# Performance work log

Hardware: AMD Instinct MI355X
Metric: run time of the kernel (lower is better)

Reference implementation:

```python
import jax, jax.numpy as jnp
import numpy as np

B = 262144          # batch of sample points
L = 16              # hash levels
T = 1 << 19         # hash table size per level
F = 2               # features per level
BASE_RES = 16
FINEST_RES = 512
DH = 64             # density MLP hidden
DOUT = 16           # density MLP out (density_out dim)
CH = 64             # color MLP hidden
PRIMES = np.array([1, 2654435761, 805459861], dtype=np.uint32)
_b = np.exp((np.log(FINEST_RES) - np.log(BASE_RES)) / (L - 1))
RES = jnp.asarray(np.floor(BASE_RES * _b ** np.arange(L)).astype(np.float32))  # (L,)


def _linear_init(key, fan_in, fan_out):
    kw, kb = jax.random.split(key)
    bound = 1.0 / np.sqrt(fan_in)
    w = jax.random.uniform(kw, (fan_in, fan_out), minval=-bound, maxval=bound)
    b = jax.random.uniform(kb, (fan_out,), minval=-bound, maxval=bound)
    return w, b


def setup_inputs() -> dict:
    key = jax.random.key(0)
    ks = jax.random.split(key, 10)
    coords = jax.random.uniform(ks[0], (B, 3), dtype=jnp.float32)          # in [0,1]
    directions = jax.random.normal(ks[1], (B, 3), dtype=jnp.float32)
    embeddings = jax.random.uniform(ks[2], (L, T, F), minval=-1e-4, maxval=1e-4, dtype=jnp.float32)
    dw1, db1 = _linear_init(ks[3], L * F, DH)
    dw2, db2 = _linear_init(ks[4], DH, DOUT)
    cw1, cb1 = _linear_init(ks[5], 16 + DOUT, CH)
    cw2, cb2 = _linear_init(ks[6], CH, CH)
    cw3, cb3 = _linear_init(ks[7], CH, CH)
    cw4, cb4 = _linear_init(ks[8], CH, 3)
    return dict(coords=coords, directions=directions, embeddings=embeddings,
                dw1=dw1, db1=db1, dw2=dw2, db2=db2,
                cw1=cw1, cb1=cb1, cw2=cw2, cb2=cb2,
                cw3=cw3, cb3=cb3, cw4=cw4, cb4=cb4)


def hash_encode(coords, embeddings):
    # coords: (B,3) in [0,1]; embeddings: (L,T,F)
    pos = coords[:, None, :] * RES[None, :, None]            # (B,L,3)
    p0 = jnp.floor(pos)
    frac = pos - p0                                           # (B,L,3)
    p0 = p0.astype(jnp.uint32)
    corners = jnp.stack([p0, p0 + jnp.uint32(1)], axis=-1)    # (B,L,3,2)
    h_ax = corners * jnp.asarray(PRIMES)[None, None, :, None]  # uint32 wraparound
    hidx = (h_ax[:, :, 0, :, None, None]
            ^ h_ax[:, :, 1, None, :, None]
            ^ h_ax[:, :, 2, None, None, :])                   # (B,L,2,2,2)
    hidx = (hidx & jnp.uint32(T - 1)).reshape(coords.shape[0], L, 8).astype(jnp.int32)
    feats = embeddings[jnp.arange(L)[None, :, None], hidx]    # (B,L,8,F)
    wx = jnp.stack([1.0 - frac[..., 0], frac[..., 0]], -1)    # (B,L,2)
    wy = jnp.stack([1.0 - frac[..., 1], frac[..., 1]], -1)
    wz = jnp.stack([1.0 - frac[..., 2], frac[..., 2]], -1)
    w = (wx[:, :, :, None, None] * wy[:, :, None, :, None] * wz[:, :, None, None, :])
    w = w.reshape(coords.shape[0], L, 8)                      # (B,L,8)
    out = jnp.sum(feats * w[..., None], axis=2)               # (B,L,F)
    return out.reshape(coords.shape[0], L * F)


def sh_encode_deg4(d):
    # d: (B,3) unit directions in [-1,1]; degree-4 real SH basis (16 comps)
    x, y, z = d[:, 0], d[:, 1], d[:, 2]
    xx, yy, zz = x * x, y * y, z * z
    xy, yz, xz = x * y, y * z, x * z
    c = jnp.full_like(x, 0.28209479177387814)
    return jnp.stack([
        c,
        -0.48860251190291987 * y,
        0.48860251190291987 * z,
        -0.48860251190291987 * x,
        1.0925484305920792 * xy,
        -1.0925484305920792 * yz,
        0.94617469575755997 * zz - 0.31539156525251999,
        -1.0925484305920792 * xz,
        0.54627421529603959 * (xx - yy),
        0.59004358992664352 * y * (-3.0 * xx + yy),
        2.8906114426405538 * xy * z,
        0.45704579946446572 * y * (1.0 - 5.0 * zz),
        0.3731763325901154 * z * (5.0 * zz - 3.0),
        0.45704579946446572 * x * (1.0 - 5.0 * zz),
        1.4453057213202769 * z * (xx - yy),
        0.59004358992664352 * x * (xx - 3.0 * yy),
    ], axis=1)


def reference(coords, directions, embeddings, dw1, db1, dw2, db2,
              cw1, cb1, cw2, cb2, cw3, cb3, cw4, cb4):
    # density net: hash encode -> Linear+ReLU -> Linear
    feat = hash_encode(coords, embeddings)                    # (B, L*F)
    h = jax.nn.relu(feat @ dw1 + db1)
    density_out = h @ dw2 + db2                               # (B, DOUT)
    density = jnp.exp(density_out[:, 0])                      # TruncExp fwd = exp
    # color net
    d = directions / jnp.linalg.norm(directions, axis=1, keepdims=True)
    d01 = (d + 1.0) / 2.0                                     # remap as in module
    sh = sh_encode_deg4(d01 * 2.0 - 1.0)                      # encoder maps back to [-1,1]
    inp = jnp.concatenate([sh, density_out], axis=1)          # (B, 32)
    x = jax.nn.relu(inp @ cw1 + cb1)
    x = jax.nn.relu(x @ cw2 + cb2)
    x = jax.nn.relu(x @ cw3 + cb3)
    color = jax.nn.sigmoid(x @ cw4 + cb4)                     # (B, 3)
    return density, color
```

## Files before the change

### kernel.cpp

```cpp
#include <hip/hip_runtime.h>
#include <cmath>

#define NPTS 262144
#define NLVL 16
#define TBL  524288u
#define TMASK 524287u
#define TPB  128

typedef __attribute__((ext_vector_type(8))) short short8;
typedef __attribute__((ext_vector_type(4))) float f32x4;

struct ResArr { float r[NLVL]; };

__device__ __forceinline__ unsigned short f2bf(float f) {
    union { float f; unsigned u; } v; v.f = f;
    unsigned r = v.u + 0x7FFFu + ((v.u >> 16) & 1u);
    return (unsigned short)(r >> 16);
}

#define MFMA(a,b,c) __builtin_amdgcn_mfma_f32_16x16x32_bf16((a),(b),(c),0,0,0)

__global__ __launch_bounds__(256) void hash_encode_k(
    const float* __restrict__ coords,
    const float* __restrict__ emb,
    unsigned* __restrict__ featws,
    ResArr res)
{
    const int b    = blockIdx.x;
    const int xcd  = b & 7;
    const int step = b >> 3;
    const int l    = (step < 1024) ? xcd : (xcd + 8);
    const int p    = (step & 1023) * 256 + threadIdx.x;

    const float cx = coords[3*p], cy = coords[3*p+1], cz = coords[3*p+2];
    const float r = res.r[l];

    const float px = cx*r, py = cy*r, pz = cz*r;
    const float fpx = floorf(px), fpy = floorf(py), fpz = floorf(pz);
    const float fx = px-fpx, fy = py-fpy, fz = pz-fpz;
    const unsigned ix=(unsigned)fpx, iy=(unsigned)fpy, iz=(unsigned)fpz;
    const unsigned hx0=ix,             hx1=ix+1u;
    const unsigned hy0=iy*2654435761u, hy1=(iy+1u)*2654435761u;
    const unsigned hz0=iz*805459861u,  hz1=(iz+1u)*805459861u;
    const unsigned base = (unsigned)l * TBL;

    const float2* __restrict__ emb2 = (const float2*)emb;
    const float2 f000 = emb2[base + ((hx0^hy0^hz0)&TMASK)];
    const float2 f001 = emb2[base + ((hx0^hy0^hz1)&TMASK)];
    const float2 f010 = emb2[base + ((hx0^hy1^hz0)&TMASK)];
    const float2 f011 = emb2[base + ((hx0^hy1^hz1)&TMASK)];
    const float2 f100 = emb2[base + ((hx1^hy0^hz0)&TMASK)];
    const float2 f101 = emb2[base + ((hx1^hy0^hz1)&TMASK)];
    const float2 f110 = emb2[base + ((hx1^hy1^hz0)&TMASK)];
    const float2 f111 = emb2[base + ((hx1^hy1^hz1)&TMASK)];

    const float wx0=1.f-fx, wy0=1.f-fy, wz0=1.f-fz;
    float o0, o1;
    o0 = wx0*wy0*wz0*f000.x;                 o1 = wx0*wy0*wz0*f000.y;
    o0 = fmaf(wx0*wy0*fz,  f001.x, o0);      o1 = fmaf(wx0*wy0*fz,  f001.y, o1);
    o0 = fmaf(wx0*fy*wz0,  f010.x, o0);      o1 = fmaf(wx0*fy*wz0,  f010.y, o1);
    o0 = fmaf(wx0*fy*fz,   f011.x, o0);      o1 = fmaf(wx0*fy*fz,   f011.y, o1);
    o0 = fmaf(fx*wy0*wz0,  f100.x, o0);      o1 = fmaf(fx*wy0*wz0,  f100.y, o1);
    o0 = fmaf(fx*wy0*fz,   f101.x, o0);      o1 = fmaf(fx*wy0*fz,   f101.y, o1);
    o0 = fmaf(fx*fy*wz0,   f110.x, o0);      o1 = fmaf(fx*fy*wz0,   f110.y, o1);
    o0 = fmaf(fx*fy*fz,    f111.x, o0);      o1 = fmaf(fx*fy*fz,    f111.y, o1);

    featws[(size_t)l * NPTS + p] = (unsigned)f2bf(o0) | ((unsigned)f2bf(o1) << 16);
}

__global__ __launch_bounds__(256, 3) void mlp_mfma_k(
    const unsigned* __restrict__ featws,
    const float* __restrict__ dirs,
    const float* __restrict__ dw1, const float* __restrict__ db1,
    const float* __restrict__ dw2, const float* __restrict__ db2,
    const float* __restrict__ cw1, const float* __restrict__ cb1,
    const float* __restrict__ cw2, const float* __restrict__ cb2,
    const float* __restrict__ cw3, const float* __restrict__ cb3,
    const float* __restrict__ cw4, const float* __restrict__ cb4,
    float* __restrict__ out)
{
    const int tid  = threadIdx.x;
    const int wid  = tid >> 6;
    const int lane = tid & 63;
    const int m16  = lane & 15;
    const int q    = lane >> 4;

    __shared__ __align__(16) unsigned short wlds[28 * 512];
    __shared__ float blds[288];
    __shared__ __align__(16) unsigned short featL[TPB * 40];
    __shared__ __align__(16) unsigned short actL[4 * 16 * 72];

    const unsigned char MAT[28] = {0,0,0,0, 1,1, 2,2,2,2, 3,3,3,3,3,3,3,3, 4,4,4,4,4,4,4,4, 5,5};
    const unsigned char K0 [28] = {0,0,0,0, 0,32, 0,0,0,0, 0,0,0,0,32,32,32,32, 0,0,0,0,32,32,32,32, 0,32};
    const unsigned char N0 [28] = {0,16,32,48, 0,0, 0,16,32,48, 0,16,32,48,0,16,32,48, 0,16,32,48,0,16,32,48, 0,0};

    #pragma unroll
    for (int s = 0; s < 28; ++s) {
        if ((s & 3) == wid) {
            const int mat = MAT[s];
            const float* src = mat==0?dw1 : mat==1?dw2 : mat==2?cw1 : mat==3?cw2 : mat==4?cw3 : cw4;
            const int fan = (mat==1) ? 16 : (mat==5) ? 3 : 64;
            const int k = (int)K0[s] + q*8;
            const int n = (int)N0[s] + m16;
            unsigned short u[8];
            #pragma unroll
            for (int j = 0; j < 8; ++j) {
                float v = 0.f;
                if (mat != 5 || n < 3) v = src[(k+j)*fan + n];
                u[j] = f2bf(v);
            }
            unsigned* w32 = (unsigned*)(wlds + s*512 + lane*8);
            w32[0] = (unsigned)u[0] | ((unsigned)u[1] << 16);
            w32[1] = (unsigned)u[2] | ((unsigned)u[3] << 16);
            w32[2] = (unsigned)u[4] | ((unsigned)u[5] << 16);
            w32[3] = (unsigned)u[6] | ((unsigned)u[7] << 16);
        }
    }
    {
        int t = tid;
        if      (t <  64) blds[t] = db1[t];
        else if (t <  80) blds[t] = db2[t-64];
        else if (t < 144) blds[t] = cb1[t-80];
        else if (t < 208) blds[t] = cb2[t-144];
    }
    if (tid < 80) {
        int t = tid + 208;
        if (t < 272) blds[t] = cb3[t-208];
        else         blds[t] = (t-272 < 3) ? cb4[t-272] : 0.f;
    }

    const int pbase = blockIdx.x * TPB;
    unsigned* fL32 = (unsigned*)featL;
    #pragma unroll
    for (int j = 0; j < 8; ++j) {
        const int idx  = j*256 + tid;
        const int l    = idx >> 7;
        const int ploc = idx & 127;
        fL32[ploc*20 + l] = featws[(size_t)l * NPTS + pbase + ploc];
    }
    __syncthreads();

    unsigned short* aw = actL + wid*1152;
    const short8* wfr = (const short8*)wlds;

    #pragma unroll
    for (int iter = 0; iter < 2; ++iter) {
        const int tile = wid + 4*iter;
        const int loc0 = tile*16;
        const int p0g  = pbase + loc0;

        short8 a0 = *(const short8*)(featL + (loc0+m16)*40 + q*8);
        f32x4 acc[4];
        #pragma unroll
        for (int nc = 0; nc < 4; ++nc) {
            const float b = blds[nc*16 + m16];
            acc[nc] = (f32x4){b,b,b,b};
            acc[nc] = MFMA(a0, wfr[nc*64 + lane], acc[nc]);
        }
        #pragma unroll
        for (int nc = 0; nc < 4; ++nc)
            #pragma unroll
            for (int r = 0; r < 4; ++r)
                aw[(q*4+r)*72 + nc*16 + m16] = f2bf(fmaxf(acc[nc][r], 0.f));

        short8 ad0 = *(const short8*)(aw + m16*72 + q*8);
        short8 ad1 = *(const short8*)(aw + m16*72 + 32 + q*8);
        f32x4 dob;
        { const float b = blds[64 + m16]; dob = (f32x4){b,b,b,b}; }
        dob = MFMA(ad0, wfr[4*64 + lane], dob);
        dob = MFMA(ad1, wfr[5*64 + lane], dob);

        if (m16 == 0) {
            #pragma unroll
            for (int r = 0; r < 4; ++r) out[p0g + q*4 + r] = expf(dob[r]);
        }

        #pragma unroll
        for (int r = 0; r < 4; ++r)
            aw[(q*4+r)*72 + 16 + m16] = f2bf(dob[r]);
        {
            const int pg = p0g + m16;
            const float dx0 = dirs[3*pg], dy0 = dirs[3*pg+1], dz0 = dirs[3*pg+2];
            const float inv = 1.f / sqrtf(dx0*dx0 + dy0*dy0 + dz0*dz0);
            float x = dx0*inv, y = dy0*inv, z = dz0*inv;
            x = ((x+1.f)*0.5f)*2.f - 1.f;
            y = ((y+1.f)*0.5f)*2.f - 1.f;
            z = ((z+1.f)*0.5f)*2.f - 1.f;
            float s0, s1, s2, s3;
            switch (q) {
            case 0: s0 = 0.28209479177387814f;
                    s1 = -0.48860251190291987f*y;
                    s2 =  0.48860251190291987f*z;
                    s3 = -0.48860251190291987f*x; break;
            case 1: s0 =  1.0925484305920792f*x*y;
                    s1 = -1.0925484305920792f*y*z;
                    s2 =  0.94617469575756f*z*z - 0.31539156525252f;
                    s3 = -1.0925484305920792f*x*z; break;
            case 2: s0 =  0.5462742152960396f*(x*x - y*y);
                    s1 =  0.5900435899266435f*y*(-3.f*x*x + y*y);
                    s2 =  2.890611442640554f*x*y*z;
                    s3 =  0.4570457994644657f*y*(1.f - 5.f*z*z); break;
            default:s0 =  0.3731763325901154f*z*(5.f*z*z - 3.f);
                    s1 =  0.4570457994644657f*x*(1.f - 5.f*z*z);
                    s2 =  1.445305721320277f*z*(x*x - y*y);
                    s3 =  0.5900435899266435f*x*(x*x - 3.f*y*y); break;
            }
            unsigned* ip = (unsigned*)(aw + m16*72 + q*4);
            ip[0] = (unsigned)f2bf(s0) | ((unsigned)f2bf(s1) << 16);
            ip[1] = (unsigned)f2bf(s2) | ((unsigned)f2bf(s3) << 16);
        }

        short8 ac0 = *(const short8*)(aw + m16*72 + q*8);
        #pragma unroll
        for (int nc = 0; nc < 4; ++nc) {
            const float b = blds[80 + nc*16 + m16];
            acc[nc] = (f32x4){b,b,b,b};
            acc[nc] = MFMA(ac0, wfr[(6+nc)*64 + lane], acc[nc]);
        }
        #pragma unroll
        for (int nc = 0; nc < 4; ++nc)
            #pragma unroll
            for (int r = 0; r < 4; ++r)
                aw[(q*4+r)*72 + nc*16 + m16] = f2bf(fmaxf(acc[nc][r], 0.f));

        short8 a20 = *(const short8*)(aw + m16*72 + q*8);
        short8 a21 = *(const short8*)(aw + m16*72 + 32 + q*8);
        #pragma unroll
        for (int nc = 0; nc < 4; ++nc) {
            const float b = blds[144 + nc*16 + m16];
            acc[nc] = (f32x4){b,b,b,b};
            acc[nc] = MFMA(a20, wfr[(10+nc)*64 + lane], acc[nc]);
            acc[nc] = MFMA(a21, wfr[(14+nc)*64 + lane], acc[nc]);
        }
        #pragma unroll
        for (int nc = 0; nc < 4; ++nc)
            #pragma unroll
            for (int r = 0; r < 4; ++r)
                aw[(q*4+r)*72 + nc*16 + m16] = f2bf(fmaxf(acc[nc][r], 0.f));

        short8 a30 = *(const short8*)(aw + m16*72 + q*8);
        short8 a31 = *(const short8*)(aw + m16*72 + 32 + q*8);
        #pragma unroll
        for (int nc = 0; nc < 4; ++nc) {
            const float b = blds[208 + nc*16 + m16];
            acc[nc] = (f32x4){b,b,b,b};
            acc[nc] = MFMA(a30, wfr[(18+nc)*64 + lane], acc[nc]);
            acc[nc] = MFMA(a31, wfr[(22+nc)*64 + lane], acc[nc]);
        }
        #pragma unroll
        for (int nc = 0; nc < 4; ++nc)
            #pragma unroll
            for (int r = 0; r < 4; ++r)
                aw[(q*4+r)*72 + nc*16 + m16] = f2bf(fmaxf(acc[nc][r], 0.f));

        short8 a40 = *(const short8*)(aw + m16*72 + q*8);
        short8 a41 = *(const short8*)(aw + m16*72 + 32 + q*8);
        f32x4 c4;
        { const float b = blds[272 + m16]; c4 = (f32x4){b,b,b,b}; }
        c4 = MFMA(a40, wfr[26*64 + lane], c4);
        c4 = MFMA(a41, wfr[27*64 + lane], c4);
        if (m16 < 3) {
            #pragma unroll
            for (int r = 0; r < 4; ++r)
                out[NPTS + 3*(p0g + q*4 + r) + m16] = 1.f / (1.f + expf(-c4[r]));
        }
    }
}

extern "C" void kernel_launch(void* const* d_in, const int* in_sizes, int n_in,
                              void* d_out, int out_size, void* d_ws, size_t ws_size,
                              hipStream_t stream)
{
    ResArr res;
    const double b = exp((log(512.0) - log(16.0)) / 15.0);
    for (int l = 0; l < NLVL; ++l)
        res.r[l] = (float)floor(16.0 * pow(b, (double)l));

    unsigned* featws = (unsigned*)d_ws;

    hash_encode_k<<<16384, 256, 0, stream>>>(
        (const float*)d_in[0],
        (const float*)d_in[2],
        featws, res);

    mlp_mfma_k<<<NPTS/TPB, 256, 0, stream>>>(
        featws,
        (const float*)d_in[1],
        (const float*)d_in[3],  (const float*)d_in[4],
        (const float*)d_in[5],  (const float*)d_in[6],
        (const float*)d_in[7],  (const float*)d_in[8],
        (const float*)d_in[9],  (const float*)d_in[10],
        (const float*)d_in[11], (const float*)d_in[12],
        (const float*)d_in[13], (const float*)d_in[14],
        (float*)d_out);
}
```

Measured before the change: 270.1 us.

## Densify coarse hash levels into linear grids for coalesced corner lookups

Adds a prepass kernel that copies the hashed embeddings for the first seven coarse levels into dense linear D^3 grids. The encoder then reads neighbouring corners from these grids, so pairs of corners sit next to each other in memory instead of being scattered by the hash. This is meant to cut scattered gather traffic and improve cache locality on the coarse levels, at the cost of an extra kernel launch, about 1.6M extra gathers and writes each call, and more workspace. Warps that handle the coarse levels take the dense branch.

```diff
diff --git a/kernel.cpp b/kernel.cpp
--- a/kernel.cpp
+++ b/kernel.cpp
@@ -6,11 +6,13 @@
 #define TBL  524288u
 #define TMASK 524287u
 #define TPB  128
+#define NDENSE 7
 
 typedef __attribute__((ext_vector_type(8))) short short8;
 typedef __attribute__((ext_vector_type(4))) float f32x4;
 
 struct ResArr { float r[NLVL]; };
+struct DenseInfo { int off[NDENSE]; int dim[NDENSE]; };
 
 __device__ __forceinline__ unsigned short f2bf(float f) {
     union { float f; unsigned u; } v; v.f = f;
@@ -20,11 +22,29 @@
 
 #define MFMA(a,b,c) __builtin_amdgcn_mfma_f32_16x16x32_bf16((a),(b),(c),0,0,0)
 
+__global__ __launch_bounds__(256) void densify_k(
+    const float* __restrict__ emb,
+    float2* __restrict__ lin,
+    DenseInfo di)
+{
+    const int l = blockIdx.y;
+    const int t = blockIdx.x * 256 + threadIdx.x;
+    const int D = di.dim[l];
+    if (t >= D*D*D) return;
+    const unsigned z = (unsigned)t % (unsigned)D;
+    const unsigned rem = (unsigned)t / (unsigned)D;
+    const unsigned y = rem % (unsigned)D;
+    const unsigned x = rem / (unsigned)D;
+    const unsigned h = (x ^ (y*2654435761u) ^ (z*805459861u)) & TMASK;
+    lin[di.off[l] + t] = ((const float2*)emb)[(unsigned)l * TBL + h];
+}
+
 __global__ __launch_bounds__(256) void hash_encode_k(
     const float* __restrict__ coords,
     const float* __restrict__ emb,
+    const float2* __restrict__ lin,
     unsigned* __restrict__ featws,
-    ResArr res)
+    ResArr res, DenseInfo di)
 {
     const int b    = blockIdx.x;
     const int xcd  = b & 7;
@@ -39,20 +59,34 @@
     const float fpx = floorf(px), fpy = floorf(py), fpz = floorf(pz);
     const float fx = px-fpx, fy = py-fpy, fz = pz-fpz;
     const unsigned ix=(unsigned)fpx, iy=(unsigned)fpy, iz=(unsigned)fpz;
-    const unsigned hx0=ix,             hx1=ix+1u;
-    const unsigned hy0=iy*2654435761u, hy1=(iy+1u)*2654435761u;
-    const unsigned hz0=iz*805459861u,  hz1=(iz+1u)*805459861u;
-    const unsigned base = (unsigned)l * TBL;
-
-    const float2* __restrict__ emb2 = (const float2*)emb;
-    const float2 f000 = emb2[base + ((hx0^hy0^hz0)&TMASK)];
-    const float2 f001 = emb2[base + ((hx0^hy0^hz1)&TMASK)];
-    const float2 f010 = emb2[base + ((hx0^hy1^hz0)&TMASK)];
-    const float2 f011 = emb2[base + ((hx0^hy1^hz1)&TMASK)];
-    const float2 f100 = emb2[base + ((hx1^hy0^hz0)&TMASK)];
-    const float2 f101 = emb2[base + ((hx1^hy0^hz1)&TMASK)];
-    const float2 f110 = emb2[base + ((hx1^hy1^hz0)&TMASK)];
-    const float2 f111 = emb2[base + ((hx1^hy1^hz1)&TMASK)];
+
+    float2 f000, f001, f010, f011, f100, f101, f110, f111;
+
+    if (l < NDENSE) {
+        const int D = di.dim[l];
+        const int v00 = ((int)ix*D + (int)iy)*D + (int)iz + di.off[l];
+        const int v01 = v00 + D;
+        const int v10 = v00 + D*D;
+        const int v11 = v10 + D;
+        f000 = lin[v00]; f001 = lin[v00+1];
+        f010 = lin[v01]; f011 = lin[v01+1];
+        f100 = lin[v10]; f101 = lin[v10+1];
+        f110 = lin[v11]; f111 = lin[v11+1];
+    } else {
+        const unsigned hx0=ix,             hx1=ix+1u;
+        const unsigned hy0=iy*2654435761u, hy1=(iy+1u)*2654435761u;
+        const unsigned hz0=iz*805459861u,  hz1=(iz+1u)*805459861u;
+        const unsigned base = (unsigned)l * TBL;
+        const float2* __restrict__ emb2 = (const float2*)emb;
+        f000 = emb2[base + ((hx0^hy0^hz0)&TMASK)];
+        f001 = emb2[base + ((hx0^hy0^hz1)&TMASK)];
+        f010 = emb2[base + ((hx0^hy1^hz0)&TMASK)];
+        f011 = emb2[base + ((hx0^hy1^hz1)&TMASK)];
+        f100 = emb2[base + ((hx1^hy0^hz0)&TMASK)];
+        f101 = emb2[base + ((hx1^hy0^hz1)&TMASK)];
+        f110 = emb2[base + ((hx1^hy1^hz0)&TMASK)];
+        f111 = emb2[base + ((hx1^hy1^hz1)&TMASK)];
+    }
 
     const float wx0=1.f-fx, wy0=1.f-fy, wz0=1.f-fz;
     float o0, o1;
@@ -276,12 +310,26 @@
     for (int l = 0; l < NLVL; ++l)
         res.r[l] = (float)floor(16.0 * pow(b, (double)l));
 
+    DenseInfo di;
+    int off = 0, maxn = 0;
+    for (int l = 0; l < NDENSE; ++l) {
+        const int D = (int)res.r[l] + 1;
+        di.dim[l] = D;
+        di.off[l] = off;
+        off += D*D*D;
+        if (D*D*D > maxn) maxn = D*D*D;
+    }
+
     unsigned* featws = (unsigned*)d_ws;
+    float2*   lin    = (float2*)((char*)d_ws + (size_t)NLVL * NPTS * 4);
+
+    densify_k<<<dim3((maxn + 255)/256, NDENSE), 256, 0, stream>>>(
+        (const float*)d_in[2], lin, di);
 
     hash_encode_k<<<16384, 256, 0, stream>>>(
         (const float*)d_in[0],
         (const float*)d_in[2],
-        featws, res);
+        lin, featws, res, di);
 
     mlp_mfma_k<<<NPTS/TPB, 256, 0, stream>>>(
         featws,
```

Result: slower. 289.0 us (+7.0%).

## Densify coarse hash levels into bf16 corner-quad grids before encoding

Applied to the files above, without the earlier changes.

Adds a pre-pass that, for the six coarsest levels, gathers the hashed embeddings into a dense grid where each cell stores the four y/z corner features as packed bf16 in one uint4. The encode kernel then reads two 16-byte loads per point for those levels instead of eight scattered float2 gathers, and each thread handles four points. The remaining levels keep the hashed path, with block-to-level mapping reworked so the grid shrinks. This adds an extra kernel launch and workspace each call, and rounds the coarse-level corner values to bf16 before interpolation.

```diff
diff --git a/kernel.cpp b/kernel.cpp
--- a/kernel.cpp
+++ b/kernel.cpp
@@ -6,66 +6,165 @@
 #define TBL  524288u
 #define TMASK 524287u
 #define TPB  128
+#define NQ   6
 
 typedef __attribute__((ext_vector_type(8))) short short8;
 typedef __attribute__((ext_vector_type(4))) float f32x4;
 
 struct ResArr { float r[NLVL]; };
+struct QuadInfo { int off[NQ]; int dim[NQ]; };
 
 __device__ __forceinline__ unsigned short f2bf(float f) {
     union { float f; unsigned u; } v; v.f = f;
     unsigned r = v.u + 0x7FFFu + ((v.u >> 16) & 1u);
     return (unsigned short)(r >> 16);
 }
+__device__ __forceinline__ float blo(unsigned u) {
+    union { unsigned v; float f; } x; x.v = u << 16; return x.f;
+}
+__device__ __forceinline__ float bhi(unsigned u) {
+    union { unsigned v; float f; } x; x.v = u & 0xffff0000u; return x.f;
+}
 
 #define MFMA(a,b,c) __builtin_amdgcn_mfma_f32_16x16x32_bf16((a),(b),(c),0,0,0)
+
+__global__ __launch_bounds__(256) void densify_quad_k(
+    const float* __restrict__ emb,
+    uint4* __restrict__ quad,
+    QuadInfo qi)
+{
+    const int l = blockIdx.y;
+    const int t = blockIdx.x * 256 + threadIdx.x;
+    const int D = qi.dim[l];
+    if (t >= D*D*D) return;
+    const unsigned z = (unsigned)t % (unsigned)D;
+    const unsigned rem = (unsigned)t / (unsigned)D;
+    const unsigned y = rem % (unsigned)D;
+    const unsigned x = rem / (unsigned)D;
+
+    const float2* __restrict__ emb2 = (const float2*)emb;
+    const unsigned base = (unsigned)l * TBL;
+    const unsigned hy0 = y*2654435761u, hy1 = (y+1u)*2654435761u;
+    const unsigned hz0 = z*805459861u,  hz1 = (z+1u)*805459861u;
+
+    const float2 a = emb2[base + ((x^hy0^hz0)&TMASK)];
+    const float2 b = emb2[base + ((x^hy0^hz1)&TMASK)];
+    const float2 c = emb2[base + ((x^hy1^hz0)&TMASK)];
+    const float2 d = emb2[base + ((x^hy1^hz1)&TMASK)];
+
+    uint4 q;
+    q.x = (unsigned)f2bf(a.x) | ((unsigned)f2bf(a.y) << 16);
+    q.y = (unsigned)f2bf(b.x) | ((unsigned)f2bf(b.y) << 16);
+    q.z = (unsigned)f2bf(c.x) | ((unsigned)f2bf(c.y) << 16);
+    q.w = (unsigned)f2bf(d.x) | ((unsigned)f2bf(d.y) << 16);
+    quad[qi.off[l] + t] = q;
+}
 
 __global__ __launch_bounds__(256) void hash_encode_k(
     const float* __restrict__ coords,
     const float* __restrict__ emb,
+    const uint4* __restrict__ quad,
     unsigned* __restrict__ featws,
-    ResArr res)
+    ResArr res, QuadInfo qi)
 {
-    const int b    = blockIdx.x;
-    const int xcd  = b & 7;
-    const int step = b >> 3;
-    const int l    = (step < 1024) ? xcd : (xcd + 8);
-    const int p    = (step & 1023) * 256 + threadIdx.x;
-
-    const float cx = coords[3*p], cy = coords[3*p+1], cz = coords[3*p+2];
-    const float r = res.r[l];
-
-    const float px = cx*r, py = cy*r, pz = cz*r;
-    const float fpx = floorf(px), fpy = floorf(py), fpz = floorf(pz);
-    const float fx = px-fpx, fy = py-fpy, fz = pz-fpz;
-    const unsigned ix=(unsigned)fpx, iy=(unsigned)fpy, iz=(unsigned)fpz;
-    const unsigned hx0=ix,             hx1=ix+1u;
-    const unsigned hy0=iy*2654435761u, hy1=(iy+1u)*2654435761u;
-    const unsigned hz0=iz*805459861u,  hz1=(iz+1u)*805459861u;
-    const unsigned base = (unsigned)l * TBL;
-
-    const float2* __restrict__ emb2 = (const float2*)emb;
-    const float2 f000 = emb2[base + ((hx0^hy0^hz0)&TMASK)];
-    const float2 f001 = emb2[base + ((hx0^hy0^hz1)&TMASK)];
-    const float2 f010 = emb2[base + ((hx0^hy1^hz0)&TMASK)];
-    const float2 f011 = emb2[base + ((hx0^hy1^hz1)&TMASK)];
-    const float2 f100 = emb2[base + ((hx1^hy0^hz0)&TMASK)];
-    const float2 f101 = emb2[base + ((hx1^hy0^hz1)&TMASK)];
-    const float2 f110 = emb2[base + ((hx1^hy1^hz0)&TMASK)];
-    const float2 f111 = emb2[base + ((hx1^hy1^hz1)&TMASK)];
-
-    const float wx0=1.f-fx, wy0=1.f-fy, wz0=1.f-fz;
-    float o0, o1;
-    o0 = wx0*wy0*wz0*f000.x;                 o1 = wx0*wy0*wz0*f000.y;
-    o0 = fmaf(wx0*wy0*fz,  f001.x, o0);      o1 = fmaf(wx0*wy0*fz,  f001.y, o1);
-    o0 = fmaf(wx0*fy*wz0,  f010.x, o0);      o1 = fmaf(wx0*fy*wz0,  f010.y, o1);
-    o0 = fmaf(wx0*fy*fz,   f011.x, o0);      o1 = fmaf(wx0*fy*fz,   f011.y, o1);
-    o0 = fmaf(fx*wy0*wz0,  f100.x, o0);      o1 = fmaf(fx*wy0*wz0,  f100.y, o1);
-    o0 = fmaf(fx*wy0*fz,   f101.x, o0);      o1 = fmaf(fx*wy0*fz,   f101.y, o1);
-    o0 = fmaf(fx*fy*wz0,   f110.x, o0);      o1 = fmaf(fx*fy*wz0,   f110.y, o1);
-    o0 = fmaf(fx*fy*fz,    f111.x, o0);      o1 = fmaf(fx*fy*fz,    f111.y, o1);
-
-    featws[(size_t)l * NPTS + p] = (unsigned)f2bf(o0) | ((unsigned)f2bf(o1) << 16);
+    const int tid = threadIdx.x;
+    const int b   = blockIdx.x;
+    const int xcd = b & 7;
+    const int s   = b >> 3;
+
+    if (s < 1024 || xcd >= 3) {
+        int l, p;
+        if (s < 1024) {
+            l = 6 + xcd;
+            p = s * 256 + tid;
+        } else {
+            if (xcd == 7) return;
+            const int u  = (s - 1024) >> 8;
+            const int c  = (s - 1024) & 255;
+            const int gq = (xcd - 3) * 2 + u;
+            l = (gq < 4) ? 14 : 15;
+            p = ((gq & 3) * 256 + c) * 256 + tid;
+        }
+
+        const float cx = coords[3*p], cy = coords[3*p+1], cz = coords[3*p+2];
+        const float r = res.r[l];
+        const float px = cx*r, py = cy*r, pz = cz*r;
+        const float fpx = floorf(px), fpy = floorf(py), fpz = floorf(pz);
+        const float fx = px-fpx, fy = py-fpy, fz = pz-fpz;
+        const unsigned ix=(unsigned)fpx, iy=(unsigned)fpy, iz=(unsigned)fpz;
+        const unsigned hx0=ix,             hx1=ix+1u;
+        const unsigned hy0=iy*2654435761u, hy1=(iy+1u)*2654435761u;
+        const unsigned hz0=iz*805459861u,  hz1=(iz+1u)*805459861u;
+        const unsigned base = (unsigned)l * TBL;
+        const float2* __restrict__ emb2 = (const float2*)emb;
+
+        const float2 f000 = emb2[base + ((hx0^hy0^hz0)&TMASK)];
+        const float2 f001 = emb2[base + ((hx0^hy0^hz1)&TMASK)];
+        const float2 f010 = emb2[base + ((hx0^hy1^hz0)&TMASK)];
+        const float2 f011 = emb2[base + ((hx0^hy1^hz1)&TMASK)];
+        const float2 f100 = emb2[base + ((hx1^hy0^hz0)&TMASK)];
+        const float2 f101 = emb2[base + ((hx1^hy0^hz1)&TMASK)];
+        const float2 f110 = emb2[base + ((hx1^hy1^hz0)&TMASK)];
+        const float2 f111 = emb2[base + ((hx1^hy1^hz1)&TMASK)];
+
+        const float wx0=1.f-fx, wy0=1.f-fy, wz0=1.f-fz;
+        float o0, o1;
+        o0 = wx0*wy0*wz0*f000.x;                 o1 = wx0*wy0*wz0*f000.y;
+        o0 = fmaf(wx0*wy0*fz,  f001.x, o0);      o1 = fmaf(wx0*wy0*fz,  f001.y, o1);
+        o0 = fmaf(wx0*fy*wz0,  f010.x, o0);      o1 = fmaf(wx0*fy*wz0,  f010.y, o1);
+        o0 = fmaf(wx0*fy*fz,   f011.x, o0);      o1 = fmaf(wx0*fy*fz,   f011.y, o1);
+        o0 = fmaf(fx*wy0*wz0,  f100.x, o0);      o1 = fmaf(fx*wy0*wz0,  f100.y, o1);
+        o0 = fmaf(fx*wy0*fz,   f101.x, o0);      o1 = fmaf(fx*wy0*fz,   f101.y, o1);
+        o0 = fmaf(fx*fy*wz0,   f110.x, o0);      o1 = fmaf(fx*fy*wz0,   f110.y, o1);
+        o0 = fmaf(fx*fy*fz,    f111.x, o0);      o1 = fmaf(fx*fy*fz,    f111.y, o1);
+
+        featws[(size_t)l * NPTS + p] = (unsigned)f2bf(o0) | ((unsigned)f2bf(o1) << 16);
+    } else {
+        const int u  = (s - 1024) >> 8;
+        const int c  = (s - 1024) & 255;
+        const int l  = 2*xcd + u;
+        const int D  = qi.dim[l];
+        const int DD = D*D;
+        const int off = qi.off[l];
+        const float r = res.r[l];
+
+        int   pidx[4];
+        uint4 qA[4], qB[4];
+        float fxa[4], fya[4], fza[4];
+        #pragma unroll
+        for (int k = 0; k < 4; ++k) {
+            const int p = c*1024 + k*256 + tid;
+            pidx[k] = p;
+            const float cx = coords[3*p], cy = coords[3*p+1], cz = coords[3*p+2];
+            const float px = cx*r, py = cy*r, pz = cz*r;
+            const float fpx = floorf(px), fpy = floorf(py), fpz = floorf(pz);
+            fxa[k] = px-fpx; fya[k] = py-fpy; fza[k] = pz-fpz;
+            const int ix=(int)fpx, iy=(int)fpy, iz=(int)fpz;
+            const int v0 = off + (ix*D + iy)*D + iz;
+            qA[k] = quad[v0];
+            qB[k] = quad[v0 + DD];
+        }
+        #pragma unroll
+        for (int k = 0; k < 4; ++k) {
+            const float fx = fxa[k], fy = fya[k], fz = fza[k];
+            const float wx0=1.f-fx, wy0=1.f-fy, wz0=1.f-fz;
+            const float w000=wx0*wy0*wz0, w001=wx0*wy0*fz;
+            const float w010=wx0*fy*wz0,  w011=wx0*fy*fz;
+            const float w100=fx*wy0*wz0,  w101=fx*wy0*fz;
+            const float w110=fx*fy*wz0,   w111=fx*fy*fz;
+            float o0, o1;
+            o0 = w000*blo(qA[k].x);              o1 = w000*bhi(qA[k].x);
+            o0 = fmaf(w001, blo(qA[k].y), o0);   o1 = fmaf(w001, bhi(qA[k].y), o1);
+            o0 = fmaf(w010, blo(qA[k].z), o0);   o1 = fmaf(w010, bhi(qA[k].z), o1);
+            o0 = fmaf(w011, blo(qA[k].w), o0);   o1 = fmaf(w011, bhi(qA[k].w), o1);
+            o0 = fmaf(w100, blo(qB[k].x), o0);   o1 = fmaf(w100, bhi(qB[k].x), o1);
+            o0 = fmaf(w101, blo(qB[k].y), o0);   o1 = fmaf(w101, bhi(qB[k].y), o1);
+            o0 = fmaf(w110, blo(qB[k].z), o0);   o1 = fmaf(w110, bhi(qB[k].z), o1);
+            o0 = fmaf(w111, blo(qB[k].w), o0);   o1 = fmaf(w111, bhi(qB[k].w), o1);
+            featws[(size_t)l * NPTS + pidx[k]] =
+                (unsigned)f2bf(o0) | ((unsigned)f2bf(o1) << 16);
+        }
+    }
 }
 
 __global__ __launch_bounds__(256, 3) void mlp_mfma_k(
@@ -276,12 +375,26 @@
     for (int l = 0; l < NLVL; ++l)
         res.r[l] = (float)floor(16.0 * pow(b, (double)l));
 
+    QuadInfo qi;
+    int off = 0, maxn = 0;
+    for (int l = 0; l < NQ; ++l) {
+        const int D = (int)res.r[l] + 1;
+        qi.dim[l] = D;
+        qi.off[l] = off;
+        off += D*D*D;
+        if (D*D*D > maxn) maxn = D*D*D;
+    }
+
     unsigned* featws = (unsigned*)d_ws;
-
-    hash_encode_k<<<16384, 256, 0, stream>>>(
+    uint4*    quad   = (uint4*)((char*)d_ws + (size_t)NLVL * NPTS * 4);
+
+    densify_quad_k<<<dim3((maxn + 255)/256, NQ), 256, 0, stream>>>(
+        (const float*)d_in[2], quad, qi);
+
+    hash_encode_k<<<12288, 256, 0, stream>>>(
         (const float*)d_in[0],
         (const float*)d_in[2],
-        featws, res);
+        quad, featws, res, qi);
 
     mlp_mfma_k<<<NPTS/TPB, 256, 0, stream>>>(
         featws,
```

After: 262.6 us. -2.8%, faster.
